# Kernel optimization log

Measured on AMD Instinct MI355X. Metric: run time of the kernel, lower is better.

Reference implementation:

```python
import jax, jax.numpy as jnp
import numpy as np

N = 40000      # nodes
E = 400000     # edges
G = 64         # graphs in batch
IN = 128       # input feature dim
D = 64         # num_hidden (per-head out dim)
H = 4          # heads per layer
C = 10         # num_classes
SLOPE = 0.2    # leaky_relu negative slope


def setup_inputs() -> dict:
    key = jax.random.key(0)
    ks = jax.random.split(key, 16)

    def p(k, shape, fan):
        return jax.random.normal(k, shape, jnp.float32) * (1.0 / np.sqrt(fan))

    x = jax.random.normal(ks[0], (N, IN), jnp.float32)
    src = jax.random.randint(ks[1], (E,), 0, N, dtype=jnp.int32)
    dst = jax.random.randint(ks[2], (E,), 0, N, dtype=jnp.int32)
    graph_id = jnp.sort(jax.random.randint(ks[3], (N,), 0, G, dtype=jnp.int32))

    W0 = p(ks[4], (IN, H * D), IN)
    al0 = p(ks[5], (H, D), D)
    ar0 = p(ks[6], (H, D), D)
    W1 = p(ks[7], (H * D, H * D), H * D)
    al1 = p(ks[8], (H, D), D)
    ar1 = p(ks[9], (H, D), D)
    W2 = p(ks[10], (H * D, H * D), H * D)
    al2 = p(ks[11], (H, D), D)
    ar2 = p(ks[12], (H, D), D)
    Wc = p(ks[13], (D, C), D)
    bc = jnp.zeros((C,), jnp.float32)
    return dict(x=x, src=src, dst=dst, graph_id=graph_id,
                W0=W0, al0=al0, ar0=ar0, W1=W1, al1=al1, ar1=ar1,
                W2=W2, al2=al2, ar2=ar2, Wc=Wc, bc=bc)


def gat_layer(h, W, al, ar, src, dst, residual, activate):
    # DGL GATConv (no bias): project, per-edge attention, edge-softmax, aggregate.
    n = h.shape[0]
    Hh, Dd = al.shape
    feat = (h @ W).reshape(n, Hh, Dd)                       # [N,H,D]
    el = jnp.einsum('nhd,hd->nh', feat, al)                 # [N,H]
    er = jnp.einsum('nhd,hd->nh', feat, ar)                 # [N,H]
    e = jax.nn.leaky_relu(el[src] + er[dst], SLOPE)         # [E,H]
    # numerically stable edge softmax over incoming edges of each dst node
    m = jax.ops.segment_max(e, dst, num_segments=n)
    m = jnp.where(jnp.isfinite(m), m, 0.0)                  # isolated nodes -> -inf
    ee = jnp.exp(e - m[dst])                                # [E,H]
    denom = jax.ops.segment_sum(ee, dst, num_segments=n)
    alpha = ee / jnp.maximum(denom[dst], 1e-9)              # [E,H]
    msg = feat[src] * alpha[..., None]                      # [E,H,D]
    out = jax.ops.segment_sum(msg, dst, num_segments=n)     # [N,H,D]
    if residual:  # identity residual (in == H*D)
        out = out + h.reshape(n, Hh, Dd)
    if activate:
        out = jax.nn.elu(out)
    return out


def reference(x, src, dst, graph_id, W0, al0, ar0, W1, al1, ar1,
              W2, al2, ar2, Wc, bc):
    h = gat_layer(x, W0, al0, ar0, src, dst, False, True).reshape(N, H * D)
    h = gat_layer(h, W1, al1, ar1, src, dst, True, True).reshape(N, H * D)
    h = gat_layer(h, W2, al2, ar2, src, dst, True, False).mean(axis=1)  # [N,D]
    # mean_nodes readout over batched graphs
    cnt = jax.ops.segment_sum(jnp.ones((N,), jnp.float32), graph_id, num_segments=G)
    hg = jax.ops.segment_sum(h, graph_id, num_segments=G) / jnp.maximum(cnt, 1.0)[:, None]
    return hg @ Wc + bc                                     # [G,C]
```

## Files before the change

kernel.cpp:

```cpp
#include <hip/hip_runtime.h>
#include <hip/hip_bf16.h>
#include <math.h>

#define N_NODES 40000
#define N_EDGES 400000
#define N_GRAPH 64
#define IN_DIM 128
#define HD 256
#define NCLS 10
#define SLOPE 0.2f

typedef __hip_bfloat16 bf16;
typedef __attribute__((ext_vector_type(8))) short short8;
typedef __attribute__((ext_vector_type(4))) float floatx4;

__device__ __forceinline__ float b2f(bf16 x){ return __bfloat162float(x); }
__device__ __forceinline__ bf16  f2b(float x){ return __float2bfloat16(x); }

__device__ __forceinline__ floatx4 unpack4(uint2 u){
  floatx4 f;
  f[0] = __uint_as_float(u.x << 16);
  f[1] = __uint_as_float(u.x & 0xffff0000u);
  f[2] = __uint_as_float(u.y << 16);
  f[3] = __uint_as_float(u.y & 0xffff0000u);
  return f;
}

__device__ __forceinline__ int wave_incl_scan(int x, int lane){
  #pragma unroll
  for (int m=1;m<64;m<<=1){
    int v = __shfl_up(x, m);
    if (lane >= m) x += v;
  }
  return x;
}

__global__ __launch_bounds__(256) void cvt_x_kernel(const float4* __restrict__ in, ushort* __restrict__ out){
  int i = blockIdx.x*256 + threadIdx.x;
  if (i >= (N_NODES*IN_DIM)/4) return;
  float4 v = in[i];
  ushort4 o;
  o.x = __bfloat16_as_ushort(f2b(v.x));
  o.y = __bfloat16_as_ushort(f2b(v.y));
  o.z = __bfloat16_as_ushort(f2b(v.z));
  o.w = __bfloat16_as_ushort(f2b(v.w));
  *(ushort4*)(out + i*4) = o;
}

__global__ __launch_bounds__(256) void cvt_w_kernel(const float* __restrict__ W, ushort* __restrict__ Wt, int K){
  int e = blockIdx.x*256 + threadIdx.x;
  if (e >= K*HD) return;
  int k = e >> 8, n = e & 255;
  float v = W[e];
  int idx = (((k>>6)*256 + n)<<6) + (k & 63);
  Wt[idx] = __bfloat16_as_ushort(f2b(v));
}

__global__ __launch_bounds__(256) void hist_kernel(const int* __restrict__ dst, int* __restrict__ cnt){
  int i = blockIdx.x*256 + threadIdx.x;
  if (i < N_EDGES) atomicAdd(&cnt[dst[i]], 1);
}

__global__ __launch_bounds__(1024) void reduce_kernel(const int* __restrict__ cnt, int* __restrict__ bsum){
  int t = threadIdx.x, b = blockIdx.x;
  int idx = b*1024 + t;
  int c = (idx < N_NODES) ? cnt[idx] : 0;
  #pragma unroll
  for (int m=32;m;m>>=1) c += __shfl_down(c, m);
  __shared__ int ws[16];
  int w = t>>6, l = t&63;
  if (l==0) ws[w] = c;
  __syncthreads();
  if (t==0){
    int s = 0;
    #pragma unroll
    for (int i=0;i<16;i++) s += ws[i];
    bsum[b] = s;
  }
}

__global__ __launch_bounds__(64) void scanb_kernel(const int* __restrict__ bsum, int* __restrict__ boff,
                                                   int* __restrict__ rs){
  int t = threadIdx.x;
  int v = (t < 40) ? bsum[t] : 0;
  int incl = wave_incl_scan(v, t);
  if (t < 40) boff[t] = incl - v;
  if (t == 39) rs[N_NODES] = incl;
}

__global__ __launch_bounds__(1024) void csr_scan_kernel(const int* __restrict__ cnt, const int* __restrict__ boff,
                                                        int* __restrict__ rs, int* __restrict__ cur){
  int t = threadIdx.x, b = blockIdx.x;
  int idx = b*1024 + t;
  int c = (idx < N_NODES) ? cnt[idx] : 0;
  int w = t>>6, l = t&63;
  int wi = wave_incl_scan(c, l);
  __shared__ int ws[16];
  __shared__ int wexcl[16];
  if (l==63) ws[w] = wi;
  __syncthreads();
  if (t < 16){
    int x = ws[t];
    #pragma unroll
    for (int m=1;m<16;m<<=1){
      int v = __shfl_up(x, m);
      if (t >= m) x += v;
    }
    wexcl[t] = x - ws[t];
  }
  __syncthreads();
  if (idx < N_NODES){
    int p = boff[b] + wexcl[w] + wi - c;
    rs[idx] = p; cur[idx] = p;
  }
}

__global__ __launch_bounds__(256) void scatter_kernel(const int* __restrict__ src, const int* __restrict__ dst,
                                                      int* __restrict__ cur, int* __restrict__ csrc){
  int i = blockIdx.x*256 + threadIdx.x;
  if (i < N_EDGES){
    int p = atomicAdd(&cur[dst[i]], 1);
    csrc[p] = src[i];
  }
}

template<int K>
__global__ __launch_bounds__(256) void gemm_kernel(const bf16* __restrict__ A, const ushort* __restrict__ Wt,
                                                   bf16* __restrict__ C,
                                                   const float* __restrict__ al, const float* __restrict__ ar,
                                                   float* __restrict__ el, float* __restrict__ er)
{
  __shared__ __align__(16) short As[64][72];
  int t = threadIdx.x;
  int lane = t & 63, w = t >> 6;
  int quad = lane >> 4, l15 = lane & 15;
  int bm = blockIdx.x;
  const ushort* Au = (const ushort*)A;
  floatx4 acc[4][4] = {};
  int srow = t >> 3, scol = (t & 7) << 3;

  for (int kc = 0; kc < K/64; ++kc){
    __syncthreads();
    #pragma unroll
    for (int i=0;i<2;++i){
      int row = srow + 32*i;
      short8 v = *(const short8*)(Au + (size_t)(bm*64 + row)*K + kc*64 + scol);
      *(short8*)&As[row][scol] = v;
    }
    __syncthreads();
    #pragma unroll
    for (int j=0;j<2;++j){
      short8 af[4], bfr[4];
      #pragma unroll
      for (int mt=0;mt<4;++mt) af[mt] = *(const short8*)&As[16*mt + l15][8*quad + 32*j];
      #pragma unroll
      for (int ct=0;ct<4;++ct){
        int n = w*64 + 16*ct + l15;
        bfr[ct] = *(const short8*)(Wt + ((size_t)(kc*256 + n)<<6) + 8*quad + 32*j);
      }
      #pragma unroll
      for (int mt=0;mt<4;++mt)
        #pragma unroll
        for (int ct=0;ct<4;++ct)
          acc[mt][ct] = __builtin_amdgcn_mfma_f32_16x16x32_bf16(af[mt], bfr[ct], acc[mt][ct], 0, 0, 0);
    }
  }

  #pragma unroll
  for (int mt=0;mt<4;++mt)
    #pragma unroll
    for (int ct=0;ct<4;++ct)
      #pragma unroll
      for (int r=0;r<4;++r){
        int row = bm*64 + 16*mt + 4*quad + r;
        C[(size_t)row*HD + w*64 + 16*ct + l15] = f2b(acc[mt][ct][r]);
      }

  float alv[4], arv[4];
  #pragma unroll
  for (int ct=0;ct<4;++ct){ alv[ct] = al[w*64 + 16*ct + l15]; arv[ct] = ar[w*64 + 16*ct + l15]; }
  #pragma unroll
  for (int mt=0;mt<4;++mt)
    #pragma unroll
    for (int r=0;r<4;++r){
      float pe = 0.f, pr_ = 0.f;
      #pragma unroll
      for (int ct=0;ct<4;++ct){ float v = acc[mt][ct][r]; pe += v*alv[ct]; pr_ += v*arv[ct]; }
      #pragma unroll
      for (int m=1;m<16;m<<=1){ pe += __shfl_xor(pe, m); pr_ += __shfl_xor(pr_, m); }
      if (l15 == 0){
        int row = bm*64 + 16*mt + 4*quad + r;
        el[row*4 + w] = pe;
        er[row*4 + w] = pr_;
      }
    }
}

__global__ __launch_bounds__(256) void agg_kernel(const bf16* __restrict__ feat,
                                                  const float* __restrict__ el, const float* __restrict__ er,
                                                  const int* __restrict__ rs, const int* __restrict__ csrc,
                                                  bf16* __restrict__ h_io,
                                                  int residual, int activate)
{
  int t = threadIdx.x;
  int w = t >> 6, l = t & 63;
  int n = blockIdx.x*4 + w;
  int h = l >> 4;
  float er_h = er[n*4 + h];
  int j0 = rs[n], j1 = rs[n+1];
  const uint2* fp = (const uint2*)feat;
  uint2* hp = (uint2*)h_io;

  floatx4 res = {0,0,0,0};
  if (residual) res = unpack4(hp[(size_t)n*64 + l]);

  floatx4 a0={0,0,0,0}, a1={0,0,0,0}, a2={0,0,0,0}, a3={0,0,0,0};
  float d0=0.f, d1=0.f, d2=0.f, d3=0.f;
  int j = j0;
  for (; j+3 < j1; j += 4){
    int s0 = csrc[j], s1 = csrc[j+1], s2 = csrc[j+2], s3 = csrc[j+3];
    float e0 = el[s0*4+h] + er_h;
    float e1 = el[s1*4+h] + er_h;
    float e2 = el[s2*4+h] + er_h;
    float e3 = el[s3*4+h] + er_h;
    e0 = (e0 > 0.f) ? e0 : SLOPE*e0;
    e1 = (e1 > 0.f) ? e1 : SLOPE*e1;
    e2 = (e2 > 0.f) ? e2 : SLOPE*e2;
    e3 = (e3 > 0.f) ? e3 : SLOPE*e3;
    float ee0 = __expf(e0), ee1 = __expf(e1), ee2 = __expf(e2), ee3 = __expf(e3);
    floatx4 f0 = unpack4(fp[(size_t)s0*64 + l]);
    floatx4 f1 = unpack4(fp[(size_t)s1*64 + l]);
    floatx4 f2 = unpack4(fp[(size_t)s2*64 + l]);
    floatx4 f3 = unpack4(fp[(size_t)s3*64 + l]);
    d0 += ee0; d1 += ee1; d2 += ee2; d3 += ee3;
    #pragma unroll
    for (int k=0;k<4;++k){
      a0[k] += ee0*f0[k]; a1[k] += ee1*f1[k];
      a2[k] += ee2*f2[k]; a3[k] += ee3*f3[k];
    }
  }
  for (; j < j1; ++j){
    int s0 = csrc[j];
    float e0 = el[s0*4+h] + er_h;
    e0 = (e0 > 0.f) ? e0 : SLOPE*e0;
    float ee0 = __expf(e0);
    floatx4 f0 = unpack4(fp[(size_t)s0*64 + l]);
    d0 += ee0;
    #pragma unroll
    for (int k=0;k<4;++k) a0[k] += ee0*f0[k];
  }
  float den = fmaxf((d0+d1)+(d2+d3), 1e-9f);
  ushort4 o;
  #pragma unroll
  for (int k=0;k<4;++k){
    float v = ((a0[k]+a1[k])+(a2[k]+a3[k])) / den + res[k];
    if (activate) v = (v > 0.f) ? v : expm1f(v);
    ((ushort*)&o)[k] = __bfloat16_as_ushort(f2b(v));
  }
  *(ushort4*)&hp[(size_t)n*64 + l] = o;
}

__global__ __launch_bounds__(256) void readout_kernel(const bf16* __restrict__ h2, const int* __restrict__ gid,
                                                      float* __restrict__ gacc, float* __restrict__ gcnt)
{
  int t = threadIdx.x;
  int w = t >> 6, l = t & 63;
  int nbase = blockIdx.x*64 + w*16;
  const uint2* hp = (const uint2*)h2;
  floatx4 run = {0,0,0,0};
  float c = 0.f;
  int curg = gid[nbase];
  for (int i=0;i<16;++i){
    int n = nbase + i;
    int g = gid[n];
    floatx4 v = unpack4(hp[(size_t)n*64 + l]);
    #pragma unroll
    for (int k=0;k<4;++k){ v[k] += __shfl_xor(v[k], 16); v[k] += __shfl_xor(v[k], 32); v[k] *= 0.25f; }
    if (g != curg){
      if (l < 16){
        #pragma unroll
        for (int k=0;k<4;++k) atomicAdd(&gacc[curg*64 + 4*l + k], run[k]);
        if (l == 0) atomicAdd(&gcnt[curg], c);
      }
      run = (floatx4){0,0,0,0}; c = 0.f; curg = g;
    }
    if (l < 16){
      #pragma unroll
      for (int k=0;k<4;++k) run[k] += v[k];
    }
    c += 1.f;
  }
  if (l < 16){
    #pragma unroll
    for (int k=0;k<4;++k) atomicAdd(&gacc[curg*64 + 4*l + k], run[k]);
    if (l == 0) atomicAdd(&gcnt[curg], c);
  }
}

__global__ __launch_bounds__(64) void classifier_kernel(const float* __restrict__ gacc, const float* __restrict__ gcnt,
                                                        const float* __restrict__ Wc, const float* __restrict__ bc,
                                                        float* __restrict__ out)
{
  int g = blockIdx.x, d = threadIdx.x;
  __shared__ float hg[64];
  hg[d] = gacc[g*64+d] / fmaxf(gcnt[g], 1.0f);
  __syncthreads();
  if (d < NCLS){
    float s = bc[d];
    #pragma unroll
    for (int k=0;k<64;k++) s += hg[k] * Wc[k*NCLS + d];
    out[g*NCLS + d] = s;
  }
}

__global__ __launch_bounds__(64) void diag_kernel(float* __restrict__ out, float v){
  int i = blockIdx.x*64 + threadIdx.x;
  if (i < N_GRAPH*NCLS) out[i] = v;
}

#define WS_NEEDED 54589216ull

extern "C" void kernel_launch(void* const* d_in, const int* in_sizes, int n_in,
                              void* d_out, int out_size, void* d_ws, size_t ws_size,
                              hipStream_t stream)
{
  (void)out_size;
  float* out = (float*)d_out;

  if (ws_size < WS_NEEDED){
    diag_kernel<<<10, 64, 0, stream>>>(out, (float)(ws_size >> 20));
    return;
  }
  static const int sz_dict[15] = {5120000,400000,400000,40000,32768,256,256,65536,256,256,65536,256,256,640,10};
  bool okd = (n_in >= 15);
  if (okd) for (int i=0;i<15;i++) if (in_sizes[i] != sz_dict[i]) { okd = false; break; }
  if (!okd){ diag_kernel<<<10, 64, 0, stream>>>(out, 3.0f); return; }

  const float* x  = (const float*)d_in[0];
  const int* src  = (const int*)d_in[1];
  const int* dst  = (const int*)d_in[2];
  const int* gid  = (const int*)d_in[3];
  const float* W0 = (const float*)d_in[4];
  const float* al0= (const float*)d_in[5];
  const float* ar0= (const float*)d_in[6];
  const float* W1 = (const float*)d_in[7];
  const float* al1= (const float*)d_in[8];
  const float* ar1= (const float*)d_in[9];
  const float* W2 = (const float*)d_in[10];
  const float* al2= (const float*)d_in[11];
  const float* ar2= (const float*)d_in[12];
  const float* Wc = (const float*)d_in[13];
  const float* bc = (const float*)d_in[14];

  char* ws = (char*)d_ws;
  int*    rs   = (int*)   (ws + 256);
  int*    csrc = (int*)   (ws + 160512);
  float*  el   = (float*) (ws + 1760512);
  float*  er   = (float*) (ws + 2400512);
  int*    cnt  = (int*)   (ws + 1760512);
  int*    cur  = (int*)   (ws + 2400512);
  bf16*   H    = (bf16*)  (ws + 3040512);
  bf16*   feat = (bf16*)  (ws + 23520512);
  float*  gacc = (float*) (ws + 44000512);
  float*  gcnt = (float*) (ws + 44016896);
  bf16*   xc   = (bf16*)  (ws + 44017152);
  ushort* Wt0  = (ushort*)(ws + 54257152);
  ushort* Wt1  = (ushort*)(ws + 54322688);
  ushort* Wt2  = (ushort*)(ws + 54453760);
  int*    bsum = (int*)   (ws + 54584832);
  int*    boff = (int*)   (ws + 54585088);

  cvt_x_kernel<<<(N_NODES*IN_DIM/4 + 255)/256, 256, 0, stream>>>((const float4*)x, (ushort*)xc);
  cvt_w_kernel<<<(IN_DIM*HD + 255)/256, 256, 0, stream>>>(W0, Wt0, IN_DIM);
  cvt_w_kernel<<<(HD*HD + 255)/256, 256, 0, stream>>>(W1, Wt1, HD);
  cvt_w_kernel<<<(HD*HD + 255)/256, 256, 0, stream>>>(W2, Wt2, HD);

  hipMemsetAsync(cnt, 0, N_NODES*sizeof(int), stream);
  hipMemsetAsync(gacc, 0, 16640, stream);

  const int eb = (N_EDGES + 255)/256;
  const int sb = (N_NODES + 1023)/1024;
  hist_kernel    <<<eb, 256, 0, stream>>>(dst, cnt);
  reduce_kernel  <<<sb, 1024, 0, stream>>>(cnt, bsum);
  scanb_kernel   <<<1, 64, 0, stream>>>(bsum, boff, rs);
  csr_scan_kernel<<<sb, 1024, 0, stream>>>(cnt, boff, rs, cur);
  scatter_kernel <<<eb, 256, 0, stream>>>(src, dst, cur, csrc);

  gemm_kernel<IN_DIM><<<625, 256, 0, stream>>>(xc, Wt0, feat, al0, ar0, el, er);
  agg_kernel<<<N_NODES/4, 256, 0, stream>>>(feat, el, er, rs, csrc, H, 0, 1);
  gemm_kernel<HD><<<625, 256, 0, stream>>>(H, Wt1, feat, al1, ar1, el, er);
  agg_kernel<<<N_NODES/4, 256, 0, stream>>>(feat, el, er, rs, csrc, H, 1, 1);
  gemm_kernel<HD><<<625, 256, 0, stream>>>(H, Wt2, feat, al2, ar2, el, er);
  agg_kernel<<<N_NODES/4, 256, 0, stream>>>(feat, el, er, rs, csrc, H, 1, 0);
  readout_kernel   <<<625, 256, 0, stream>>>(H, gid, gacc, gcnt);
  classifier_kernel<<<N_GRAPH, 64, 0, stream>>>(gacc, gcnt, Wc, bc, out);
}
```

Before: 357.8 us.

## Merge prep kernels, fold block scan into CSR scan, cooperatively load edge indices

Merges the x and weight conversions and the workspace zeroing into one multi-role prep kernel. It also folds the per-graph node count into the histogram kernel and moves the block-offset scan inside the CSR scan kernel. Together these remove several kernel launches and two memsets. In aggregation, each wave now loads up to 64 edge source indices at once and broadcasts them with shuffles instead of having every lane load each index. The cost is more branching inside the combined kernels and a redundant small scan run in every CSR-scan block.

```diff
diff --git a/kernel.cpp b/kernel.cpp
--- a/kernel.cpp
+++ b/kernel.cpp
@@ -35,30 +35,56 @@
   return x;
 }
 
-__global__ __launch_bounds__(256) void cvt_x_kernel(const float4* __restrict__ in, ushort* __restrict__ out){
-  int i = blockIdx.x*256 + threadIdx.x;
-  if (i >= (N_NODES*IN_DIM)/4) return;
-  float4 v = in[i];
-  ushort4 o;
-  o.x = __bfloat16_as_ushort(f2b(v.x));
-  o.y = __bfloat16_as_ushort(f2b(v.y));
-  o.z = __bfloat16_as_ushort(f2b(v.z));
-  o.w = __bfloat16_as_ushort(f2b(v.w));
-  *(ushort4*)(out + i*4) = o;
-}
-
-__global__ __launch_bounds__(256) void cvt_w_kernel(const float* __restrict__ W, ushort* __restrict__ Wt, int K){
-  int e = blockIdx.x*256 + threadIdx.x;
-  if (e >= K*HD) return;
-  int k = e >> 8, n = e & 255;
-  float v = W[e];
-  int idx = (((k>>6)*256 + n)<<6) + (k & 63);
-  Wt[idx] = __bfloat16_as_ushort(f2b(v));
-}
-
-__global__ __launch_bounds__(256) void hist_kernel(const int* __restrict__ dst, int* __restrict__ cnt){
-  int i = blockIdx.x*256 + threadIdx.x;
-  if (i < N_EDGES) atomicAdd(&cnt[dst[i]], 1);
+__global__ __launch_bounds__(256) void prep_kernel(const float4* __restrict__ x4, ushort* __restrict__ xc,
+                                                   const float* __restrict__ W0, ushort* __restrict__ Wt0,
+                                                   const float* __restrict__ W1, ushort* __restrict__ Wt1,
+                                                   const float* __restrict__ W2, ushort* __restrict__ Wt2,
+                                                   int* __restrict__ cnt, float* __restrict__ gacc,
+                                                   int* __restrict__ gcnt)
+{
+  int b = blockIdx.x, t = threadIdx.x;
+  if (b < 5000){
+    int i = b*256 + t;
+    float4 v = x4[i];
+    ushort4 o;
+    o.x = __bfloat16_as_ushort(f2b(v.x));
+    o.y = __bfloat16_as_ushort(f2b(v.y));
+    o.z = __bfloat16_as_ushort(f2b(v.z));
+    o.w = __bfloat16_as_ushort(f2b(v.w));
+    *(ushort4*)(xc + i*4) = o;
+  } else if (b < 5640){
+    const float* W; ushort* Wt; int e0, n_el;
+    if (b < 5128){ W = W0; Wt = Wt0; e0 = (b-5000)*256; n_el = IN_DIM*HD; }
+    else if (b < 5384){ W = W1; Wt = Wt1; e0 = (b-5128)*256; n_el = HD*HD; }
+    else { W = W2; Wt = Wt2; e0 = (b-5384)*256; n_el = HD*HD; }
+    int e = e0 + t;
+    if (e < n_el){
+      int k = e >> 8, n = e & 255;
+      int idx = (((k>>6)*256 + n)<<6) + (k & 63);
+      Wt[idx] = __bfloat16_as_ushort(f2b(W[e]));
+    }
+  } else if (b < 5797){
+    int i = (b-5640)*256 + t;
+    if (i < N_NODES) cnt[i] = 0;
+  } else {
+    #pragma unroll
+    for (int k=0;k<16;++k) gacc[t*16 + k] = 0.f;
+    if (t < N_GRAPH) gcnt[t] = 0;
+  }
+}
+
+#define EB 1563
+#define GB 157
+__global__ __launch_bounds__(256) void hist_kernel(const int* __restrict__ dst, int* __restrict__ cnt,
+                                                   const int* __restrict__ gid, int* __restrict__ gcnt){
+  int b = blockIdx.x;
+  if (b < EB){
+    int i = b*256 + threadIdx.x;
+    if (i < N_EDGES) atomicAdd(&cnt[dst[i]], 1);
+  } else {
+    int i = (b-EB)*256 + threadIdx.x;
+    if (i < N_NODES) atomicAdd(&gcnt[gid[i]], 1);
+  }
 }
 
 __global__ __launch_bounds__(1024) void reduce_kernel(const int* __restrict__ cnt, int* __restrict__ bsum){
@@ -79,18 +105,16 @@
   }
 }
 
-__global__ __launch_bounds__(64) void scanb_kernel(const int* __restrict__ bsum, int* __restrict__ boff,
-                                                   int* __restrict__ rs){
-  int t = threadIdx.x;
-  int v = (t < 40) ? bsum[t] : 0;
-  int incl = wave_incl_scan(v, t);
-  if (t < 40) boff[t] = incl - v;
-  if (t == 39) rs[N_NODES] = incl;
-}
-
-__global__ __launch_bounds__(1024) void csr_scan_kernel(const int* __restrict__ cnt, const int* __restrict__ boff,
+__global__ __launch_bounds__(1024) void csr_scan_kernel(const int* __restrict__ cnt, const int* __restrict__ bsum,
                                                         int* __restrict__ rs, int* __restrict__ cur){
   int t = threadIdx.x, b = blockIdx.x;
+  __shared__ int boff_s;
+  if (t < 64){
+    int v = (t < 40) ? bsum[t] : 0;
+    int incl = wave_incl_scan(v, t);
+    if (t == b) boff_s = incl - v;
+    if (b == 39 && t == 39) rs[N_NODES] = incl;
+  }
   int idx = b*1024 + t;
   int c = (idx < N_NODES) ? cnt[idx] : 0;
   int w = t>>6, l = t&63;
@@ -110,7 +134,7 @@
   }
   __syncthreads();
   if (idx < N_NODES){
-    int p = boff[b] + wexcl[w] + wi - c;
+    int p = boff_s + wexcl[w] + wi - c;
     rs[idx] = p; cur[idx] = p;
   }
 }
@@ -216,38 +240,44 @@
 
   floatx4 a0={0,0,0,0}, a1={0,0,0,0}, a2={0,0,0,0}, a3={0,0,0,0};
   float d0=0.f, d1=0.f, d2=0.f, d3=0.f;
-  int j = j0;
-  for (; j+3 < j1; j += 4){
-    int s0 = csrc[j], s1 = csrc[j+1], s2 = csrc[j+2], s3 = csrc[j+3];
-    float e0 = el[s0*4+h] + er_h;
-    float e1 = el[s1*4+h] + er_h;
-    float e2 = el[s2*4+h] + er_h;
-    float e3 = el[s3*4+h] + er_h;
-    e0 = (e0 > 0.f) ? e0 : SLOPE*e0;
-    e1 = (e1 > 0.f) ? e1 : SLOPE*e1;
-    e2 = (e2 > 0.f) ? e2 : SLOPE*e2;
-    e3 = (e3 > 0.f) ? e3 : SLOPE*e3;
-    float ee0 = __expf(e0), ee1 = __expf(e1), ee2 = __expf(e2), ee3 = __expf(e3);
-    floatx4 f0 = unpack4(fp[(size_t)s0*64 + l]);
-    floatx4 f1 = unpack4(fp[(size_t)s1*64 + l]);
-    floatx4 f2 = unpack4(fp[(size_t)s2*64 + l]);
-    floatx4 f3 = unpack4(fp[(size_t)s3*64 + l]);
-    d0 += ee0; d1 += ee1; d2 += ee2; d3 += ee3;
-    #pragma unroll
-    for (int k=0;k<4;++k){
-      a0[k] += ee0*f0[k]; a1[k] += ee1*f1[k];
-      a2[k] += ee2*f2[k]; a3[k] += ee3*f3[k];
-    }
-  }
-  for (; j < j1; ++j){
-    int s0 = csrc[j];
-    float e0 = el[s0*4+h] + er_h;
-    e0 = (e0 > 0.f) ? e0 : SLOPE*e0;
-    float ee0 = __expf(e0);
-    floatx4 f0 = unpack4(fp[(size_t)s0*64 + l]);
-    d0 += ee0;
-    #pragma unroll
-    for (int k=0;k<4;++k) a0[k] += ee0*f0[k];
+
+  for (int base = j0; base < j1; base += 64){
+    int m = j1 - base; if (m > 64) m = 64;
+    int eidx = csrc[base + (l < m ? l : m-1)];
+    int jj = 0;
+    for (; jj+3 < m; jj += 4){
+      int s0 = __shfl(eidx, jj),   s1 = __shfl(eidx, jj+1);
+      int s2 = __shfl(eidx, jj+2), s3 = __shfl(eidx, jj+3);
+      float e0 = el[s0*4+h] + er_h;
+      float e1 = el[s1*4+h] + er_h;
+      float e2 = el[s2*4+h] + er_h;
+      float e3 = el[s3*4+h] + er_h;
+      e0 = (e0 > 0.f) ? e0 : SLOPE*e0;
+      e1 = (e1 > 0.f) ? e1 : SLOPE*e1;
+      e2 = (e2 > 0.f) ? e2 : SLOPE*e2;
+      e3 = (e3 > 0.f) ? e3 : SLOPE*e3;
+      float ee0 = __expf(e0), ee1 = __expf(e1), ee2 = __expf(e2), ee3 = __expf(e3);
+      floatx4 f0 = unpack4(fp[(size_t)s0*64 + l]);
+      floatx4 f1 = unpack4(fp[(size_t)s1*64 + l]);
+      floatx4 f2 = unpack4(fp[(size_t)s2*64 + l]);
+      floatx4 f3 = unpack4(fp[(size_t)s3*64 + l]);
+      d0 += ee0; d1 += ee1; d2 += ee2; d3 += ee3;
+      #pragma unroll
+      for (int k=0;k<4;++k){
+        a0[k] += ee0*f0[k]; a1[k] += ee1*f1[k];
+        a2[k] += ee2*f2[k]; a3[k] += ee3*f3[k];
+      }
+    }
+    for (; jj < m; ++jj){
+      int s0 = __shfl(eidx, jj);
+      float e0 = el[s0*4+h] + er_h;
+      e0 = (e0 > 0.f) ? e0 : SLOPE*e0;
+      float ee0 = __expf(e0);
+      floatx4 f0 = unpack4(fp[(size_t)s0*64 + l]);
+      d0 += ee0;
+      #pragma unroll
+      for (int k=0;k<4;++k) a0[k] += ee0*f0[k];
+    }
   }
   float den = fmaxf((d0+d1)+(d2+d3), 1e-9f);
   ushort4 o;
@@ -261,14 +291,13 @@
 }
 
 __global__ __launch_bounds__(256) void readout_kernel(const bf16* __restrict__ h2, const int* __restrict__ gid,
-                                                      float* __restrict__ gacc, float* __restrict__ gcnt)
+                                                      float* __restrict__ gacc)
 {
   int t = threadIdx.x;
   int w = t >> 6, l = t & 63;
   int nbase = blockIdx.x*64 + w*16;
   const uint2* hp = (const uint2*)h2;
   floatx4 run = {0,0,0,0};
-  float c = 0.f;
   int curg = gid[nbase];
   for (int i=0;i<16;++i){
     int n = nbase + i;
@@ -280,30 +309,27 @@
       if (l < 16){
         #pragma unroll
         for (int k=0;k<4;++k) atomicAdd(&gacc[curg*64 + 4*l + k], run[k]);
-        if (l == 0) atomicAdd(&gcnt[curg], c);
       }
-      run = (floatx4){0,0,0,0}; c = 0.f; curg = g;
+      run = (floatx4){0,0,0,0}; curg = g;
     }
     if (l < 16){
       #pragma unroll
       for (int k=0;k<4;++k) run[k] += v[k];
     }
-    c += 1.f;
   }
   if (l < 16){
     #pragma unroll
     for (int k=0;k<4;++k) atomicAdd(&gacc[curg*64 + 4*l + k], run[k]);
-    if (l == 0) atomicAdd(&gcnt[curg], c);
-  }
-}
-
-__global__ __launch_bounds__(64) void classifier_kernel(const float* __restrict__ gacc, const float* __restrict__ gcnt,
+  }
+}
+
+__global__ __launch_bounds__(64) void classifier_kernel(const float* __restrict__ gacc, const int* __restrict__ gcnt,
                                                         const float* __restrict__ Wc, const float* __restrict__ bc,
                                                         float* __restrict__ out)
 {
   int g = blockIdx.x, d = threadIdx.x;
   __shared__ float hg[64];
-  hg[d] = gacc[g*64+d] / fmaxf(gcnt[g], 1.0f);
+  hg[d] = gacc[g*64+d] / fmaxf((float)gcnt[g], 1.0f);
   __syncthreads();
   if (d < NCLS){
     float s = bc[d];
@@ -362,28 +388,21 @@
   bf16*   H    = (bf16*)  (ws + 3040512);
   bf16*   feat = (bf16*)  (ws + 23520512);
   float*  gacc = (float*) (ws + 44000512);
-  float*  gcnt = (float*) (ws + 44016896);
+  int*    gcnt = (int*)   (ws + 44016896);
   bf16*   xc   = (bf16*)  (ws + 44017152);
   ushort* Wt0  = (ushort*)(ws + 54257152);
   ushort* Wt1  = (ushort*)(ws + 54322688);
   ushort* Wt2  = (ushort*)(ws + 54453760);
   int*    bsum = (int*)   (ws + 54584832);
-  int*    boff = (int*)   (ws + 54585088);
-
-  cvt_x_kernel<<<(N_NODES*IN_DIM/4 + 255)/256, 256, 0, stream>>>((const float4*)x, (ushort*)xc);
-  cvt_w_kernel<<<(IN_DIM*HD + 255)/256, 256, 0, stream>>>(W0, Wt0, IN_DIM);
-  cvt_w_kernel<<<(HD*HD + 255)/256, 256, 0, stream>>>(W1, Wt1, HD);
-  cvt_w_kernel<<<(HD*HD + 255)/256, 256, 0, stream>>>(W2, Wt2, HD);
-
-  hipMemsetAsync(cnt, 0, N_NODES*sizeof(int), stream);
-  hipMemsetAsync(gacc, 0, 16640, stream);
+
+  prep_kernel<<<5798, 256, 0, stream>>>((const float4*)x, (ushort*)xc,
+                                        W0, Wt0, W1, Wt1, W2, Wt2, cnt, gacc, gcnt);
 
   const int eb = (N_EDGES + 255)/256;
   const int sb = (N_NODES + 1023)/1024;
-  hist_kernel    <<<eb, 256, 0, stream>>>(dst, cnt);
+  hist_kernel    <<<EB + GB, 256, 0, stream>>>(dst, cnt, gid, gcnt);
   reduce_kernel  <<<sb, 1024, 0, stream>>>(cnt, bsum);
-  scanb_kernel   <<<1, 64, 0, stream>>>(bsum, boff, rs);
-  csr_scan_kernel<<<sb, 1024, 0, stream>>>(cnt, boff, rs, cur);
+  csr_scan_kernel<<<sb, 1024, 0, stream>>>(cnt, bsum, rs, cur);
   scatter_kernel <<<eb, 256, 0, stream>>>(src, dst, cur, csrc);
 
   gemm_kernel<IN_DIM><<<625, 256, 0, stream>>>(xc, Wt0, feat, al0, ar0, el, er);
@@ -392,6 +411,6 @@
   agg_kernel<<<N_NODES/4, 256, 0, stream>>>(feat, el, er, rs, csrc, H, 1, 1);
   gemm_kernel<HD><<<625, 256, 0, stream>>>(H, Wt2, feat, al2, ar2, el, er);
   agg_kernel<<<N_NODES/4, 256, 0, stream>>>(feat, el, er, rs, csrc, H, 1, 0);
-  readout_kernel   <<<625, 256, 0, stream>>>(H, gid, gacc, gcnt);
+  readout_kernel   <<<625, 256, 0, stream>>>(H, gid, gacc);
   classifier_kernel<<<N_GRAPH, 64, 0, stream>>>(gacc, gcnt, Wc, bc, out);
 }
```

Result: slower. 524.4 us (+46.6%).
